# Kernel tuning notes

Measured on AMD Instinct MI355X. Metric: run time of the kernel, lower is better.

The kernel has to match this reference:

```python
import jax, jax.numpy as jnp
import numpy as np

B, L, D_MODEL, N_HEADS = 8, 256, 2048, 8
D_HEAD = D_MODEL // N_HEADS  # 256 == L, required by DeltaRuleOperator broadcasting
ALPHA0, BETA0 = 0.1, 0.9      # delta_rule_strength, 1 - strength
LN_EPS = 1e-5


def setup_inputs() -> dict:
    k = jax.random.key(0)
    ks = jax.random.split(k, 8)
    s = 0.02
    return {
        "query": jax.random.normal(ks[0], (B, L, D_MODEL), jnp.float32),
        "key": jax.random.normal(ks[1], (B, L, D_MODEL), jnp.float32),
        "value": jax.random.normal(ks[2], (B, L, D_MODEL), jnp.float32),
        "Wq": jax.random.normal(ks[3], (D_MODEL, D_MODEL), jnp.float32) * s,
        "Wk": jax.random.normal(ks[4], (D_MODEL, D_MODEL), jnp.float32) * s,
        "Wv": jax.random.normal(ks[5], (D_MODEL, D_MODEL), jnp.float32) * s,
        "Wo": jax.random.normal(ks[6], (D_MODEL, D_MODEL), jnp.float32) * s,
        "bo": jnp.zeros((D_MODEL,), jnp.float32),
        "ln_g": jnp.ones((D_MODEL,), jnp.float32),
        "ln_b": jnp.zeros((D_MODEL,), jnp.float32),
        "alpha": jnp.asarray(ALPHA0, jnp.float32),
        "beta": jnp.asarray(BETA0, jnp.float32),
    }


def reference(query, key, value, Wq, Wk, Wv, Wo, bo, ln_g, ln_b, alpha, beta):
    Bs, Ls, D = query.shape
    H, Dh = N_HEADS, D // N_HEADS

    def proj(x, W):  # torch Linear: x @ W.T, split heads -> [B,H,L,Dh]
        return (x @ W.T).reshape(Bs, Ls, H, Dh).transpose(0, 2, 1, 3)

    Q = proj(query, Wq)
    K = proj(key, Wk)
    V = proj(value, Wv)

    # DeltaRuleOperator, applied sequentially per head (buffer mutates across heads)
    kv = jnp.einsum('bhld,bhmd->bhlm', K, V)  # [B,H,L,L] with L == Dh
    kv_heads = jnp.moveaxis(kv, 1, 0)          # [H,B,L,L]

    def cs_step(cs, kv_h):
        # cumulative_state = beta*cs + alpha*detach(mean(kv)); head uses pre-update cs
        new = beta * cs + alpha * jax.lax.stop_gradient(kv_h.mean(axis=(0, 1)))
        return new, cs

    _, cs_seq = jax.lax.scan(cs_step, jnp.zeros((Dh,), query.dtype), kv_heads)  # [H,Dh]
    cs_b = cs_seq[None, :, None, :]                       # [1,H,1,Dh]
    q_mod = Q * (cs_b + alpha * (kv - cs_b))              # delta-rule modulated queries

    # elu feature map
    phi = lambda x: jax.nn.elu(x) + 1.0
    pq, pk = phi(q_mod), phi(K)

    def time_major(x):  # [B,H,L,Dh] -> [L, B*H, Dh]
        return x.reshape(Bs * H, Ls, Dh).transpose(1, 0, 2)

    pq_t, pk_t, v_t = time_major(pq), time_major(pk), time_major(V)

    def step(carry, xs):
        S, Z = carry                        # S:[N,Dh,Dh], Z:[N,Dh]
        q_i, k_i, v_i = xs                  # each [N,Dh]
        S = S + k_i[:, :, None] * v_i[:, None, :]
        Z = Z + k_i
        num = jnp.einsum('nf,nfd->nd', q_i, S)
        den = jnp.maximum(jnp.sum(q_i * Z, axis=-1), 1e-8)
        return (S, Z), num / den[:, None]

    N = Bs * H
    S0 = jnp.zeros((N, Dh, Dh), query.dtype)
    Z0 = jnp.zeros((N, Dh), query.dtype)
    _, outs = jax.lax.scan(step, (S0, Z0), (pq_t, pk_t, v_t))  # [L,N,Dh]

    attn = outs.transpose(1, 0, 2).reshape(Bs, H, Ls, Dh)
    attn = attn.transpose(0, 2, 1, 3).reshape(Bs, Ls, D)       # concat heads

    o = attn @ Wo.T + bo                  # out_proj (dropout is identity in eval)
    x = query + o                          # residual + LayerNorm
    mu = x.mean(-1, keepdims=True)
    var = jnp.mean((x - mu) ** 2, axis=-1, keepdims=True)
    return (x - mu) / jnp.sqrt(var + LN_EPS) * ln_g + ln_b
```

## Files before the change

### kernel.cpp

```cpp
#include <hip/hip_runtime.h>
#include <hip/hip_bf16.h>

using u16 = unsigned short;

typedef __bf16 bf16x8 __attribute__((ext_vector_type(8)));
typedef float  f32x4  __attribute__((ext_vector_type(4)));

typedef __attribute__((address_space(1))) void gas_void;
typedef __attribute__((address_space(3))) void las_void;

__device__ __forceinline__ float b2f(u16 u) {
  union { unsigned u; float f; } v; v.u = ((unsigned)u) << 16; return v.f;
}
__device__ __forceinline__ u16 f2b(float f) {
  union { float f; unsigned u; } v; v.f = f;
  unsigned r = v.u + 0x7fffu + ((v.u >> 16) & 1u);
  return (u16)(r >> 16);
}

__device__ __forceinline__ void gld_lds16(const u16* g, u16* l) {
  __builtin_amdgcn_global_load_lds((gas_void*)g, (las_void*)l, 16, 0, 0);
}

template <int EPI, int BK>
__global__ __launch_bounds__(256) void gemm_bt(
    const u16* __restrict__ A, int lda, long sA1, long sA2,
    const u16* __restrict__ B, int ldb, long sB1, long sB2,
    void* __restrict__ Cv, int ldc, long sC1, long sC2,
    int K, int HDIV,
    const float* __restrict__ bias, const float* __restrict__ resid,
    float* __restrict__ partOut) {
  __shared__ __align__(16) u16 lds[2 * 128 * BK];
  __shared__ float denS[128];
  const int t = threadIdx.x;
  const int lane = t & 63;
  const int wave = t >> 6;
  const int wm = wave >> 1, wn = wave & 1;
  const int laneM = lane & 15, quad = lane >> 4;
  const int zb = blockIdx.z / HDIV, zh = blockIdx.z % HDIV;

  int bx = blockIdx.x, by = blockIdx.y;
  if (EPI == 2) { by = (bx >= 1) ? 1 : 0; bx = (bx == 2) ? 1 : 0; }
  const int kEnd = (EPI == 3) ? ((by + 1) * 128 < K ? (by + 1) * 128 : K) : K;

  const u16* Abase = A + zb * sA1 + zh * sA2 + (long)by * 128 * lda;
  const u16* Bbase = B + zb * sB1 + zh * sB2 + (long)bx * 128 * ldb;

  constexpr int STEPS = BK / 16;
  constexpr int RPS = 2048 / BK;
  constexpr int KK = BK / 32;
  const int sRow = (BK == 64) ? (t >> 3) : (t >> 2);
  const int sg = (BK == 64) ? (t & 7) : (t & 3);
  const int swz = (BK == 64) ? (sg ^ (sRow & 7)) : (sg ^ ((sRow >> 1) & 3));
  const int sc = swz * 8;

  f32x4 acc[4][4];
#pragma unroll
  for (int i = 0; i < 4; ++i)
#pragma unroll
    for (int j = 0; j < 4; ++j) acc[i][j] = (f32x4){0.f, 0.f, 0.f, 0.f};
  float dsum[4] = {0.f, 0.f, 0.f, 0.f};

  for (int k0 = 0; k0 < kEnd; k0 += BK) {
#pragma unroll
    for (int p = 0; p < STEPS; ++p)
      gld_lds16(Abase + (long)(p * RPS + sRow) * lda + k0 + sc,
                &lds[p * 2048 + t * 8]);
#pragma unroll
    for (int p = 0; p < STEPS; ++p)
      gld_lds16(Bbase + (long)(p * RPS + sRow) * ldb + k0 + sc,
                &lds[128 * BK + p * 2048 + t * 8]);
    __syncthreads();
    bf16x8 af[KK][4], bfv[KK][4];
#pragma unroll
    for (int kk = 0; kk < KK; ++kk) {
      int perm8;
      if (BK == 64) perm8 = ((kk * 4 + quad) ^ (laneM & 7)) * 8;
      else          perm8 = (quad ^ ((laneM >> 1) & 3)) * 8;
#pragma unroll
      for (int i = 0; i < 4; ++i) {
        af[kk][i] = *(const bf16x8*)&lds[(wm * 64 + i * 16 + laneM) * BK + perm8];
        bfv[kk][i] =
            *(const bf16x8*)&lds[128 * BK + (wn * 64 + i * 16 + laneM) * BK + perm8];
      }
    }
    if (EPI == 3) {
#pragma unroll
      for (int kk = 0; kk < KK; ++kk)
#pragma unroll
        for (int i = 0; i < 4; ++i) {
          union { bf16x8 v; u16 s[8]; } u; u.v = af[kk][i];
          float ds = 0.f;
#pragma unroll
          for (int e = 0; e < 8; ++e) ds += b2f(u.s[e]);
          dsum[i] += ds;
        }
    }
#pragma unroll
    for (int kk = 0; kk < KK; ++kk)
#pragma unroll
      for (int i = 0; i < 4; ++i)
#pragma unroll
        for (int j = 0; j < 4; ++j)
          acc[i][j] = __builtin_amdgcn_mfma_f32_16x16x32_bf16(
              af[kk][i], bfv[kk][j], acc[i][j], 0, 0, 0);
    __syncthreads();
  }

  if (EPI == 3) {
#pragma unroll
    for (int i = 0; i < 4; ++i) {
      float s = dsum[i];
      s += __shfl_xor(s, 16);
      s += __shfl_xor(s, 32);
      if (wn == 0 && quad == 0)
        denS[wm * 64 + i * 16 + laneM] = fmaxf(s, 1e-8f);
    }
    __syncthreads();
  }

  if (EPI == 1) {
#pragma unroll
    for (int j = 0; j < 4; ++j) {
      float s = 0.f;
#pragma unroll
      for (int i = 0; i < 4; ++i)
#pragma unroll
        for (int r = 0; r < 4; ++r) s += acc[i][j][r];
      s += __shfl_xor(s, 16);
      s += __shfl_xor(s, 32);
      if (quad == 0)
        atomicAdd(&partOut[zh * 256 + bx * 128 + wn * 64 + j * 16 + laneM], s);
    }
  }

  const long cOff = zb * sC1 + zh * sC2;
  const int colB = bx * 128 + wn * 64;
#pragma unroll
  for (int i = 0; i < 4; ++i) {
#pragma unroll
    for (int j = 0; j < 4; ++j) {
#pragma unroll
      for (int r = 0; r < 4; ++r) {
        const int lrow = wm * 64 + i * 16 + quad * 4 + r;
        const int row = by * 128 + lrow;
        const int col = colB + j * 16 + laneM;
        const long idx = cOff + (long)row * ldc + col;
        float v = acc[i][j][r];
        if (EPI == 0 || EPI == 1) {
          ((u16*)Cv)[idx] = f2b(v);
        } else if (EPI == 2) {
          ((u16*)Cv)[idx] = f2b(col <= row ? v : 0.0f);
        } else if (EPI == 3) {
          ((u16*)Cv)[idx] = f2b(v / denS[lrow]);
        } else {
          ((float*)Cv)[idx] =
              (zb == 0) ? v + bias[col] + resid[(long)row * ldc + col] : v;
        }
      }
    }
  }
}

__device__ __forceinline__ void g256_tile(
    const u16* __restrict__ la, const u16* __restrict__ lb,
    u16* __restrict__ sa, u16* __restrict__ sb, int tau, int nt,
    const u16* AgR0, const u16* AgR1, const u16* BgR0, const u16* BgR1,
    int rowA, int rowB, int rg, int t, f32x4 (&acc)[8][4]) {
  const bool st = (tau + 3) < nt;
  const int ks = (tau + 3) << 5;
  bf16x8 af[4], bv[4];
#pragma unroll
  for (int m = 0; m < 4; ++m)
    af[m] = *(const bf16x8*)&la[(rowA + m * 16) * 32 + rg];
#pragma unroll
  for (int n = 0; n < 4; ++n)
    bv[n] = *(const bf16x8*)&lb[(rowB + n * 16) * 32 + rg];
  if (st) {
    gld_lds16(AgR0 + ks, &sa[t * 8]);
    gld_lds16(AgR1 + ks, &sa[4096 + t * 8]);
  }
  __builtin_amdgcn_s_barrier();
  asm volatile("s_waitcnt lgkmcnt(0)" ::: "memory");
  __builtin_amdgcn_s_setprio(1);
#pragma unroll
  for (int m = 0; m < 4; ++m)
#pragma unroll
    for (int n = 0; n < 4; ++n)
      acc[m][n] = __builtin_amdgcn_mfma_f32_16x16x32_bf16(af[m], bv[n],
                                                          acc[m][n], 0, 0, 0);
  __builtin_amdgcn_s_setprio(0);
  __builtin_amdgcn_s_barrier();
#pragma unroll
  for (int m = 0; m < 4; ++m)
    af[m] = *(const bf16x8*)&la[(rowA + 64 + m * 16) * 32 + rg];
  if (st) {
    gld_lds16(BgR0 + ks, &sb[t * 8]);
    gld_lds16(BgR1 + ks, &sb[4096 + t * 8]);
  }
  __builtin_amdgcn_s_barrier();
  asm volatile("s_waitcnt lgkmcnt(0)" ::: "memory");
  __builtin_amdgcn_s_setprio(1);
#pragma unroll
  for (int m = 0; m < 4; ++m)
#pragma unroll
    for (int n = 0; n < 4; ++n)
      acc[4 + m][n] = __builtin_amdgcn_mfma_f32_16x16x32_bf16(
          af[m], bv[n], acc[4 + m][n], 0, 0, 0);
  __builtin_amdgcn_s_setprio(0);
  if (tau < nt - 1) {
    if (tau + 3 < nt)
      asm volatile("s_waitcnt vmcnt(8)" ::: "memory");
    else if (tau + 2 < nt)
      asm volatile("s_waitcnt vmcnt(4)" ::: "memory");
    else
      asm volatile("s_waitcnt vmcnt(0)" ::: "memory");
    __builtin_amdgcn_s_barrier();
  }
}

template <int EPI>
__global__ __launch_bounds__(512) void gemm256(
    const u16* __restrict__ A, int lda, long sA1,
    const u16* __restrict__ B, int ldb, long sB1,
    void* __restrict__ Cv, int ldc, long sC1, int K,
    const float* __restrict__ bias, const float* __restrict__ resid) {
  __shared__ __align__(16) u16 A0[8192], A1[8192], A2[8192], A3[8192];
  __shared__ __align__(16) u16 B0[8192], B1[8192], B2[8192], B3[8192];
  const int t = threadIdx.x;
  const int lane = t & 63, wave = t >> 6;
  const int wm = wave >> 2, wn = wave & 3;
  const int laneM = lane & 15, quad = lane >> 4;

  const int cpx = gridDim.x >> 3;
  const int id2 = (blockIdx.x & 7) * cpx + (blockIdx.x >> 3);
  const int bx = id2 & 7, by = (id2 >> 3) & 7, z = id2 >> 6;

  const u16* Ag = A + (long)z * sA1 + (long)by * 256 * lda;
  const u16* Bg = B + (long)z * sB1 + (long)bx * 256 * ldb;

  const int nt = K >> 5;
  const int rg = (quad ^ ((laneM >> 1) & 3)) * 8;
  const int rowA = wm * 128 + laneM;
  const int rowB = wn * 64 + laneM;

  const int sRow0 = t >> 2, sRow1 = (512 + t) >> 2;
  const int sc0 = (((t) & 3) ^ ((sRow0 >> 1) & 3)) * 8;
  const int sc1 = (((512 + t) & 3) ^ ((sRow1 >> 1) & 3)) * 8;
  const u16* AgR0 = Ag + (long)sRow0 * lda + sc0;
  const u16* AgR1 = Ag + (long)sRow1 * lda + sc1;
  const u16* BgR0 = Bg + (long)sRow0 * ldb + sc0;
  const u16* BgR1 = Bg + (long)sRow1 * ldb + sc1;

  f32x4 acc[8][4];
#pragma unroll
  for (int i = 0; i < 8; ++i)
#pragma unroll
    for (int j = 0; j < 4; ++j) acc[i][j] = (f32x4){0.f, 0.f, 0.f, 0.f};

  gld_lds16(AgR0, &A0[t * 8]);      gld_lds16(AgR1, &A0[4096 + t * 8]);
  gld_lds16(BgR0, &B0[t * 8]);      gld_lds16(BgR1, &B0[4096 + t * 8]);
  gld_lds16(AgR0 + 32, &A1[t * 8]); gld_lds16(AgR1 + 32, &A1[4096 + t * 8]);
  gld_lds16(BgR0 + 32, &B1[t * 8]); gld_lds16(BgR1 + 32, &B1[4096 + t * 8]);
  gld_lds16(AgR0 + 64, &A2[t * 8]); gld_lds16(AgR1 + 64, &A2[4096 + t * 8]);
  gld_lds16(BgR0 + 64, &B2[t * 8]); gld_lds16(BgR1 + 64, &B2[4096 + t * 8]);
  asm volatile("s_waitcnt vmcnt(8)" ::: "memory");
  __builtin_amdgcn_s_barrier();

  for (int tau = 0; tau < nt; tau += 4) {
    g256_tile(A0, B0, A3, B3, tau, nt, AgR0, AgR1, BgR0, BgR1, rowA, rowB,
              rg, t, acc);
    g256_tile(A1, B1, A0, B0, tau + 1, nt, AgR0, AgR1, BgR0, BgR1, rowA,
              rowB, rg, t, acc);
    g256_tile(A2, B2, A1, B1, tau + 2, nt, AgR0, AgR1, BgR0, BgR1, rowA,
              rowB, rg, t, acc);
    g256_tile(A3, B3, A2, B2, tau + 3, nt, AgR0, AgR1, BgR0, BgR1, rowA,
              rowB, rg, t, acc);
  }

  const long cOff = (long)z * sC1;
  const int colB = bx * 256 + wn * 64;
  const int rowBase = by * 256 + wm * 128;
#pragma unroll
  for (int i = 0; i < 8; ++i) {
#pragma unroll
    for (int j = 0; j < 4; ++j) {
#pragma unroll
      for (int r = 0; r < 4; ++r) {
        const int row = rowBase + i * 16 + quad * 4 + r;
        const int col = colB + j * 16 + laneM;
        const long idx = cOff + (long)row * ldc + col;
        float v = acc[i][j][r];
        if (EPI == 0) {
          ((u16*)Cv)[idx] = f2b(v);
        } else {
          ((float*)Cv)[idx] =
              (z == 0) ? v + bias[col] + resid[(long)row * ldc + col] : v;
        }
      }
    }
  }
}

__global__ __launch_bounds__(256) void convert7(
    const float* __restrict__ s0, const float* __restrict__ s1,
    const float* __restrict__ s2, const float* __restrict__ s3,
    const float* __restrict__ s4, const float* __restrict__ s5,
    const float* __restrict__ s6, u16* __restrict__ dst) {
  long idx = (long)blockIdx.x * 256 + threadIdx.x;
  int seg = (int)(idx >> 20);
  long off = (idx & 1048575) << 2;
  const float* s;
  switch (seg) {
    case 0: s = s0; break; case 1: s = s1; break; case 2: s = s2; break;
    case 3: s = s3; break; case 4: s = s4; break; case 5: s = s5; break;
    default: s = s6;
  }
  float4 v = *(const float4*)(s + off);
  ushort4 o;
  o.x = f2b(v.x); o.y = f2b(v.y); o.z = f2b(v.z); o.w = f2b(v.w);
  *(ushort4*)(dst + (long)seg * 4194304 + off) = o;
}

__global__ __launch_bounds__(256) void cs_kernel(
    const float* __restrict__ part, float* __restrict__ cs,
    const float* __restrict__ alphaP, const float* __restrict__ betaP) {
  int m = threadIdx.x;
  float alpha = *alphaP, beta = *betaP;
  float c = 0.f;
  for (int h = 0; h < 8; ++h) {
    cs[h * 256 + m] = c;
    c = beta * c + alpha * (part[h * 256 + m] * (1.0f / 2048.0f));
  }
}

__global__ __launch_bounds__(256) void pqpk_kernel(
    const u16* __restrict__ Qp, const u16* __restrict__ Kp,
    const u16* __restrict__ kv, const float* __restrict__ cs,
    const float* __restrict__ alphaP, u16* __restrict__ pq,
    u16* __restrict__ pk) {
  long idx = (long)blockIdx.x * 256 + threadIdx.x;
  int d = idx & 255, l = (int)((idx >> 8) & 255), h = (int)((idx >> 16) & 7),
      b = (int)(idx >> 19);
  float alpha = *alphaP;
  long pidx = ((long)(b * 256 + l)) * 2048 + h * 256 + d;
  float Qv = b2f(Qp[pidx]);
  float kvv = b2f(kv[idx]);
  float csv = cs[h * 256 + d];
  float qm = Qv * (csv + alpha * (kvv - csv));
  pq[idx] = f2b(qm > 0.f ? qm + 1.f : expf(qm));
  float Kv = b2f(Kp[pidx]);
  pk[idx] = f2b(Kv > 0.f ? Kv + 1.f : expf(Kv));
}

__global__ __launch_bounds__(256) void vtrans_kernel(const u16* __restrict__ Vp,
                                                     u16* __restrict__ Vt) {
  __shared__ u16 tile[32][33];
  int z = blockIdx.z, b = z >> 3, h = z & 7;
  int jT = blockIdx.x * 32, dT = blockIdx.y * 32;
  int tx = threadIdx.x, ty = threadIdx.y;
#pragma unroll
  for (int ii = 0; ii < 4; ++ii) {
    int j = jT + ty + ii * 8, d = dT + tx;
    tile[ty + ii * 8][tx] = Vp[(long)(b * 256 + j) * 2048 + h * 256 + d];
  }
  __syncthreads();
#pragma unroll
  for (int ii = 0; ii < 4; ++ii) {
    int d = dT + ty + ii * 8, j = jT + tx;
    Vt[(long)z * 65536 + d * 256 + j] = tile[tx][ty + ii * 8];
  }
}

__global__ __launch_bounds__(256) void ln_kernel(
    const float* __restrict__ x0, const float* __restrict__ x1,
    const float* __restrict__ g, const float* __restrict__ bb,
    float* __restrict__ out) {
  int row = blockIdx.x, t = threadIdx.x;
  const float4* xr0 = (const float4*)(x0 + (long)row * 2048);
  const float4* xr1 = (const float4*)(x1 + (long)row * 2048);
  float4 a0 = xr0[t], b0 = xr1[t], a1 = xr0[t + 256], b1 = xr1[t + 256];
  float4 v0, v1;
  v0.x = a0.x + b0.x; v0.y = a0.y + b0.y; v0.z = a0.z + b0.z; v0.w = a0.w + b0.w;
  v1.x = a1.x + b1.x; v1.y = a1.y + b1.y; v1.z = a1.z + b1.z; v1.w = a1.w + b1.w;
  float s = v0.x + v0.y + v0.z + v0.w + v1.x + v1.y + v1.z + v1.w;
  float ss = v0.x * v0.x + v0.y * v0.y + v0.z * v0.z + v0.w * v0.w +
             v1.x * v1.x + v1.y * v1.y + v1.z * v1.z + v1.w * v1.w;
  for (int o = 32; o; o >>= 1) { s += __shfl_xor(s, o); ss += __shfl_xor(ss, o); }
  __shared__ float a1s[4], a2s[4];
  int wave = t >> 6, lane = t & 63;
  if (lane == 0) { a1s[wave] = s; a2s[wave] = ss; }
  __syncthreads();
  s = a1s[0] + a1s[1] + a1s[2] + a1s[3];
  ss = a2s[0] + a2s[1] + a2s[2] + a2s[3];
  float mu = s * (1.f / 2048.f);
  float var = ss * (1.f / 2048.f) - mu * mu;
  float rstd = rsqrtf(var + 1e-5f);
  const float4* g4 = (const float4*)g;
  const float4* b4 = (const float4*)bb;
  float4* orow = (float4*)(out + (long)row * 2048);
  float4 gg = g4[t], bv = b4[t], r;
  r.x = (v0.x - mu) * rstd * gg.x + bv.x;
  r.y = (v0.y - mu) * rstd * gg.y + bv.y;
  r.z = (v0.z - mu) * rstd * gg.z + bv.z;
  r.w = (v0.w - mu) * rstd * gg.w + bv.w;
  orow[t] = r;
  gg = g4[t + 256]; bv = b4[t + 256];
  r.x = (v1.x - mu) * rstd * gg.x + bv.x;
  r.y = (v1.y - mu) * rstd * gg.y + bv.y;
  r.z = (v1.z - mu) * rstd * gg.z + bv.z;
  r.w = (v1.w - mu) * rstd * gg.w + bv.w;
  orow[t + 256] = r;
}

extern "C" void kernel_launch(void* const* d_in, const int* in_sizes, int n_in,
                              void* d_out, int out_size, void* d_ws,
                              size_t ws_size, hipStream_t stream) {
  const float* query = (const float*)d_in[0];
  const float* key = (const float*)d_in[1];
  const float* value = (const float*)d_in[2];
  const float* Wq = (const float*)d_in[3];
  const float* Wk = (const float*)d_in[4];
  const float* Wv = (const float*)d_in[5];
  const float* Wo = (const float*)d_in[6];
  const float* bo = (const float*)d_in[7];
  const float* ln_g = (const float*)d_in[8];
  const float* ln_b = (const float*)d_in[9];
  const float* alphaP = (const float*)d_in[10];
  const float* betaP = (const float*)d_in[11];

  char* ws = (char*)d_ws;
  const long SZ = 8388608;
  u16* qb = (u16*)(ws);
  u16* Wb = (u16*)(ws + 3 * SZ);
  u16* Qp = (u16*)(ws + 7 * SZ);
  u16* kvb = (u16*)(ws + 10 * SZ);
  u16* pq = (u16*)(ws + 12 * SZ);
  u16* pk = (u16*)(ws + 13 * SZ);
  u16* Vt = (u16*)(ws + 14 * SZ);
  u16* attnb = (u16*)(ws + 15 * SZ);
  u16* Ab = (u16*)(ws + 10 * SZ);
  float* x0 = (float*)(ws + 12 * SZ);
  float* x1 = (float*)(ws);
  float* part = (float*)(ws + 16 * SZ);
  float* cs = (float*)(ws + 16 * SZ + 16384);

  u16* Kp = Qp + 4194304;
  u16* Vp = Qp + 8388608;
  u16* Wob = Wb + 3 * 4194304;

  hipMemsetAsync(part, 0, 8 * 256 * sizeof(float), stream);

  convert7<<<28672, 256, 0, stream>>>(query, key, value, Wq, Wk, Wv, Wo, qb);

  gemm256<0><<<dim3(192, 1, 1), 512, 0, stream>>>(
      qb, 2048, 4194304L, Wb, 2048, 4194304L, (void*)Qp, 2048, 4194304L,
      2048, nullptr, nullptr);

  gemm_bt<1, 64><<<dim3(2, 2, 64), 256, 0, stream>>>(
      Kp, 2048, 524288L, 256L, Vp, 2048, 524288L, 256L, (void*)kvb, 256,
      524288L, 65536L, 256, 8, nullptr, nullptr, part);

  cs_kernel<<<1, 256, 0, stream>>>(part, cs, alphaP, betaP);

  pqpk_kernel<<<16384, 256, 0, stream>>>(Qp, Kp, kvb, cs, alphaP, pq, pk);

  gemm_bt<2, 64><<<dim3(3, 1, 64), 256, 0, stream>>>(
      pq, 256, 524288L, 65536L, pk, 256, 524288L, 65536L, (void*)Ab, 256,
      524288L, 65536L, 256, 8, nullptr, nullptr, nullptr);

  vtrans_kernel<<<dim3(8, 8, 64), dim3(32, 8), 0, stream>>>(Vp, Vt);

  gemm_bt<3, 64><<<dim3(2, 2, 64), 256, 0, stream>>>(
      Ab, 256, 524288L, 65536L, Vt, 256, 524288L, 65536L, (void*)attnb, 2048,
      524288L, 256L, 256, 8, nullptr, nullptr, nullptr);

  gemm256<4><<<dim3(128, 1, 1), 512, 0, stream>>>(
      attnb, 2048, 1024L, Wob, 2048, 1024L, (void*)x0, 2048, -25165824L,
      1024, bo, query);

  ln_kernel<<<2048, 256, 0, stream>>>(x0, x1, ln_g, ln_b, (float*)d_out);
}
```

Before: 340.1 us.

## Software-pipeline LDS fragment loads in gemm256 and vectorize pqpk elementwise kernel

The 256x256 GEMM main loop now prefetches the next k-tile's A/B register fragments from LDS while the current MFMAs run. It ping-pongs between two register sets and drops the per-tile s_barrier pairs in favour of partial lgkmcnt waits. Separately, the pq/pk feature-map kernel processes 8 elements per thread with vector loads and stores, and launches 8x fewer blocks. Removing the barriers and tightening the vmcnt counts raises register pressure and risks LDS read/write races if the wait counts are off.

Result: slower. 553.9 us (+62.9%).

```diff
diff --git a/kernel.cpp b/kernel.cpp
--- a/kernel.cpp
+++ b/kernel.cpp
@@ -163,55 +163,62 @@
 }
 
 __device__ __forceinline__ void g256_tile(
-    const u16* __restrict__ la, const u16* __restrict__ lb,
-    u16* __restrict__ sa, u16* __restrict__ sb, int tau, int nt,
+    const u16* __restrict__ lc,
+    const u16* __restrict__ lnA,
+    const u16* __restrict__ lnB,
+    u16* __restrict__ sa, u16* __restrict__ sb,
+    int tau, int nt,
     const u16* AgR0, const u16* AgR1, const u16* BgR0, const u16* BgR1,
-    int rowA, int rowB, int rg, int t, f32x4 (&acc)[8][4]) {
+    int rowA, int rowB, int rg, int t,
+    bf16x8 (&aIn)[4], bf16x8 (&bIn)[4],
+    bf16x8 (&aOut)[4], bf16x8 (&bOut)[4],
+    f32x4 (&acc)[8][4]) {
   const bool st = (tau + 3) < nt;
   const int ks = (tau + 3) << 5;
-  bf16x8 af[4], bv[4];
-#pragma unroll
-  for (int m = 0; m < 4; ++m)
-    af[m] = *(const bf16x8*)&la[(rowA + m * 16) * 32 + rg];
-#pragma unroll
-  for (int n = 0; n < 4; ++n)
-    bv[n] = *(const bf16x8*)&lb[(rowB + n * 16) * 32 + rg];
   if (st) {
     gld_lds16(AgR0 + ks, &sa[t * 8]);
     gld_lds16(AgR1 + ks, &sa[4096 + t * 8]);
   }
-  __builtin_amdgcn_s_barrier();
-  asm volatile("s_waitcnt lgkmcnt(0)" ::: "memory");
+  bf16x8 aH1[4];
+#pragma unroll
+  for (int m = 0; m < 4; ++m)
+    aH1[m] = *(const bf16x8*)&lc[(rowA + 64 + m * 16) * 32 + rg];
+  asm volatile("s_waitcnt lgkmcnt(4)" ::: "memory");
+  __builtin_amdgcn_sched_barrier(0);
   __builtin_amdgcn_s_setprio(1);
 #pragma unroll
   for (int m = 0; m < 4; ++m)
 #pragma unroll
     for (int n = 0; n < 4; ++n)
-      acc[m][n] = __builtin_amdgcn_mfma_f32_16x16x32_bf16(af[m], bv[n],
+      acc[m][n] = __builtin_amdgcn_mfma_f32_16x16x32_bf16(aIn[m], bIn[n],
                                                           acc[m][n], 0, 0, 0);
   __builtin_amdgcn_s_setprio(0);
-  __builtin_amdgcn_s_barrier();
-#pragma unroll
-  for (int m = 0; m < 4; ++m)
-    af[m] = *(const bf16x8*)&la[(rowA + 64 + m * 16) * 32 + rg];
   if (st) {
     gld_lds16(BgR0 + ks, &sb[t * 8]);
     gld_lds16(BgR1 + ks, &sb[4096 + t * 8]);
   }
-  __builtin_amdgcn_s_barrier();
-  asm volatile("s_waitcnt lgkmcnt(0)" ::: "memory");
+  if (tau + 1 < nt) {
+#pragma unroll
+    for (int m = 0; m < 4; ++m)
+      aOut[m] = *(const bf16x8*)&lnA[(rowA + m * 16) * 32 + rg];
+#pragma unroll
+    for (int n = 0; n < 4; ++n)
+      bOut[n] = *(const bf16x8*)&lnB[(rowB + n * 16) * 32 + rg];
+    asm volatile("s_waitcnt lgkmcnt(8)" ::: "memory");
+  } else {
+    asm volatile("s_waitcnt lgkmcnt(0)" ::: "memory");
+  }
+  __builtin_amdgcn_sched_barrier(0);
   __builtin_amdgcn_s_setprio(1);
 #pragma unroll
   for (int m = 0; m < 4; ++m)
 #pragma unroll
     for (int n = 0; n < 4; ++n)
       acc[4 + m][n] = __builtin_amdgcn_mfma_f32_16x16x32_bf16(
-          af[m], bv[n], acc[4 + m][n], 0, 0, 0);
+          aH1[m], bIn[n], acc[4 + m][n], 0, 0, 0);
   __builtin_amdgcn_s_setprio(0);
   if (tau < nt - 1) {
     if (tau + 3 < nt)
-      asm volatile("s_waitcnt vmcnt(8)" ::: "memory");
-    else if (tau + 2 < nt)
       asm volatile("s_waitcnt vmcnt(4)" ::: "memory");
     else
       asm volatile("s_waitcnt vmcnt(0)" ::: "memory");
@@ -264,18 +271,26 @@
   gld_lds16(BgR0 + 32, &B1[t * 8]); gld_lds16(BgR1 + 32, &B1[4096 + t * 8]);
   gld_lds16(AgR0 + 64, &A2[t * 8]); gld_lds16(AgR1 + 64, &A2[4096 + t * 8]);
   gld_lds16(BgR0 + 64, &B2[t * 8]); gld_lds16(BgR1 + 64, &B2[4096 + t * 8]);
-  asm volatile("s_waitcnt vmcnt(8)" ::: "memory");
+  asm volatile("s_waitcnt vmcnt(4)" ::: "memory");
   __builtin_amdgcn_s_barrier();
 
+  bf16x8 aP[4], bP[4], aQ[4], bQ[4];
+#pragma unroll
+  for (int m = 0; m < 4; ++m)
+    aP[m] = *(const bf16x8*)&A0[(rowA + m * 16) * 32 + rg];
+#pragma unroll
+  for (int n = 0; n < 4; ++n)
+    bP[n] = *(const bf16x8*)&B0[(rowB + n * 16) * 32 + rg];
+
   for (int tau = 0; tau < nt; tau += 4) {
-    g256_tile(A0, B0, A3, B3, tau, nt, AgR0, AgR1, BgR0, BgR1, rowA, rowB,
-              rg, t, acc);
-    g256_tile(A1, B1, A0, B0, tau + 1, nt, AgR0, AgR1, BgR0, BgR1, rowA,
-              rowB, rg, t, acc);
-    g256_tile(A2, B2, A1, B1, tau + 2, nt, AgR0, AgR1, BgR0, BgR1, rowA,
-              rowB, rg, t, acc);
-    g256_tile(A3, B3, A2, B2, tau + 3, nt, AgR0, AgR1, BgR0, BgR1, rowA,
-              rowB, rg, t, acc);
+    g256_tile(A0, A1, B1, A3, B3, tau + 0, nt, AgR0, AgR1, BgR0, BgR1,
+              rowA, rowB, rg, t, aP, bP, aQ, bQ, acc);
+    g256_tile(A1, A2, B2, A0, B0, tau + 1, nt, AgR0, AgR1, BgR0, BgR1,
+              rowA, rowB, rg, t, aQ, bQ, aP, bP, acc);
+    g256_tile(A2, A3, B3, A1, B1, tau + 2, nt, AgR0, AgR1, BgR0, BgR1,
+              rowA, rowB, rg, t, aP, bP, aQ, bQ, acc);
+    g256_tile(A3, A0, B0, A2, B2, tau + 3, nt, AgR0, AgR1, BgR0, BgR1,
+              rowA, rowB, rg, t, aQ, bQ, aP, bP, acc);
   }
 
   const long cOff = (long)z * sC1;
@@ -339,18 +354,35 @@
     const u16* __restrict__ kv, const float* __restrict__ cs,
     const float* __restrict__ alphaP, u16* __restrict__ pq,
     u16* __restrict__ pk) {
-  long idx = (long)blockIdx.x * 256 + threadIdx.x;
-  int d = idx & 255, l = (int)((idx >> 8) & 255), h = (int)((idx >> 16) & 7),
-      b = (int)(idx >> 19);
+  long base = ((long)blockIdx.x * 256 + threadIdx.x) * 8;
+  int d0 = (int)(base & 255), l = (int)((base >> 8) & 255),
+      h = (int)((base >> 16) & 7), b = (int)(base >> 19);
   float alpha = *alphaP;
-  long pidx = ((long)(b * 256 + l)) * 2048 + h * 256 + d;
-  float Qv = b2f(Qp[pidx]);
-  float kvv = b2f(kv[idx]);
-  float csv = cs[h * 256 + d];
-  float qm = Qv * (csv + alpha * (kvv - csv));
-  pq[idx] = f2b(qm > 0.f ? qm + 1.f : expf(qm));
-  float Kv = b2f(Kp[pidx]);
-  pk[idx] = f2b(Kv > 0.f ? Kv + 1.f : expf(Kv));
+  long pidx = ((long)(b * 256 + l)) * 2048 + h * 256 + d0;
+  ushort4 q0 = *(const ushort4*)(Qp + pidx);
+  ushort4 q1 = *(const ushort4*)(Qp + pidx + 4);
+  ushort4 k0 = *(const ushort4*)(Kp + pidx);
+  ushort4 k1 = *(const ushort4*)(Kp + pidx + 4);
+  ushort4 v0 = *(const ushort4*)(kv + base);
+  ushort4 v1 = *(const ushort4*)(kv + base + 4);
+  float4 c0 = *(const float4*)(cs + h * 256 + d0);
+  float4 c1 = *(const float4*)(cs + h * 256 + d0 + 4);
+  u16 qs[8] = {q0.x, q0.y, q0.z, q0.w, q1.x, q1.y, q1.z, q1.w};
+  u16 ks[8] = {k0.x, k0.y, k0.z, k0.w, k1.x, k1.y, k1.z, k1.w};
+  u16 vs[8] = {v0.x, v0.y, v0.z, v0.w, v1.x, v1.y, v1.z, v1.w};
+  float cf[8] = {c0.x, c0.y, c0.z, c0.w, c1.x, c1.y, c1.z, c1.w};
+  u16 oq[8], ok[8];
+#pragma unroll
+  for (int e = 0; e < 8; ++e) {
+    float qm = b2f(qs[e]) * (cf[e] + alpha * (b2f(vs[e]) - cf[e]));
+    oq[e] = f2b(qm > 0.f ? qm + 1.f : expf(qm));
+    float Kv = b2f(ks[e]);
+    ok[e] = f2b(Kv > 0.f ? Kv + 1.f : expf(Kv));
+  }
+  *(ushort4*)(pq + base) = (ushort4){oq[0], oq[1], oq[2], oq[3]};
+  *(ushort4*)(pq + base + 4) = (ushort4){oq[4], oq[5], oq[6], oq[7]};
+  *(ushort4*)(pk + base) = (ushort4){ok[0], ok[1], ok[2], ok[3]};
+  *(ushort4*)(pk + base + 4) = (ushort4){ok[4], ok[5], ok[6], ok[7]};
 }
 
 __global__ __launch_bounds__(256) void vtrans_kernel(const u16* __restrict__ Vp,
@@ -463,7 +495,7 @@
 
   cs_kernel<<<1, 256, 0, stream>>>(part, cs, alphaP, betaP);
 
-  pqpk_kernel<<<16384, 256, 0, stream>>>(Qp, Kp, kvb, cs, alphaP, pq, pk);
+  pqpk_kernel<<<2048, 256, 0, stream>>>(Qp, Kp, kvb, cs, alphaP, pq, pk);
 
   gemm_bt<2, 64><<<dim3(3, 1, 64), 256, 0, stream>>>(
       pq, 256, 524288L, 65536L, pk, 256, 524288L, 65536L, (void*)Ab, 256,
```
